# Optimization experiments

Measured on AMD Instinct MI355X. Metric: run time of the kernel, lower is better.

Reference implementation:

```python
import jax, jax.numpy as jnp
import numpy as np


def conv1x1(x, w, b):
    # x: [B,C,H,W], w: [O,C], b: [O] -> [B,O,H,W]
    return jnp.einsum('bchw,oc->bohw', x, w) + b[None, :, None, None]


def setup_inputs() -> dict:
    key = jax.random.key(0)
    ks = jax.random.split(key, 8)
    B, H, W = 32, 64, 64
    PoI_N, PT_feat, T_feat = 128, 64, 32
    poi = jax.random.uniform(ks[0], (B, PoI_N, H, W), dtype=jnp.float32)
    time = jax.random.normal(ks[1], (B, 31, H, W), dtype=jnp.float32)
    s = 0.05
    wm = jax.random.normal(ks[2], (T_feat, 31), dtype=jnp.float32) * s
    bm = jnp.zeros((T_feat,), jnp.float32)
    wf = jax.random.normal(ks[3], (1, T_feat), dtype=jnp.float32) * s
    bf = jnp.zeros((1,), jnp.float32)
    wc = jax.random.normal(ks[4], (PT_feat, PoI_N), dtype=jnp.float32) * s
    bc = jnp.zeros((PT_feat,), jnp.float32)
    return {'poi': poi, 'time': time, 'wm': wm, 'bm': bm, 'wf': wf, 'bf': bf, 'wc': wc, 'bc': bc}


def reference(poi, time, wm, bm, wf, bf, wc, bc):
    # Time_trans: conv1x1 -> relu -> conv1x1 -> relu, out channels = 1
    z = jax.nn.relu(conv1x1(time, wm, bm))
    T_x = jax.nn.relu(conv1x1(z, wf, bf))  # [B,1,H,W]
    # original does a detached CPU tile/multiply: broadcast multiply, no grad through it
    poi_time = jax.lax.stop_gradient(T_x * poi)  # [B,PoI_N,H,W]
    return conv1x1(poi_time, wc, bc)
```

## Files before the change

kernel.cpp:

```cpp
#include <hip/hip_runtime.h>
#include <hip/hip_bf16.h>

typedef short bf16x8 __attribute__((ext_vector_type(8)));
typedef float f32x4  __attribute__((ext_vector_type(4)));
typedef unsigned int u32;
typedef unsigned int u32x4 __attribute__((ext_vector_type(4)));

constexpr int HW = 4096;
constexpr int CT = 31;
constexpr int CZ = 32;
constexpr int CP = 128;
constexpr int CO = 64;

__device__ __forceinline__ u32 f2bfu(float x) {
    __hip_bfloat16 h = __float2bfloat16(x);
    return (u32)*reinterpret_cast<unsigned short*>(&h);
}

__global__ __launch_bounds__(256)
void time_mlp2(const float* __restrict__ tin,
               const float* __restrict__ wm,
               const float* __restrict__ bm,
               const float* __restrict__ wf,
               const float* __restrict__ bf,
               float* __restrict__ tbuf)
{
    const int gid = blockIdx.x * 256 + threadIdx.x;
    const int px  = gid * 2;
    const int b   = px >> 12;
    const float* tp = tin + (size_t)b * CT * HW + (px & (HW - 1));

    float2 tr[CT];
    #pragma unroll
    for (int c = 0; c < CT; ++c)
        tr[c] = *reinterpret_cast<const float2*>(tp + (size_t)c * HW);
    __builtin_amdgcn_sched_barrier(0);

    float ax = bf[0], ay = ax;
    #pragma unroll
    for (int k = 0; k < CZ; ++k) {
        float zx = bm[k], zy = zx;
        #pragma unroll
        for (int c = 0; c < CT; ++c) {
            const float w = wm[k * CT + c];
            zx = fmaf(w, tr[c].x, zx);
            zy = fmaf(w, tr[c].y, zy);
        }
        const float wk = wf[k];
        ax = fmaf(wk, fmaxf(zx, 0.f), ax);
        ay = fmaf(wk, fmaxf(zy, 0.f), ay);
    }
    float2 r; r.x = fmaxf(ax, 0.f); r.y = fmaxf(ay, 0.f);
    *reinterpret_cast<float2*>(tbuf + px) = r;
}

__global__ __launch_bounds__(256)
void poi_gemm_lds(const float* __restrict__ poi,
                  const float* __restrict__ tbuf,
                  const float* __restrict__ wc,
                  const float* __restrict__ bc,
                  float* __restrict__ out)
{
    __shared__ __align__(16) unsigned short s_poi[64 * CP];

    const int tid  = threadIdx.x;
    const int lane = tid & 63;
    const int m    = lane & 15;
    const int g    = lane >> 4;
    const int wid  = tid >> 6;
    const int b    = blockIdx.x >> 6;
    const int px0  = (blockIdx.x & 63) << 6;

    bf16x8 wcf[4];
    #pragma unroll
    for (int kf = 0; kf < 4; ++kf)
      #pragma unroll
      for (int j = 0; j < 8; ++j)
        wcf[kf][j] = (short)f2bfu(wc[(wid * 16 + m) * CP + kf * 32 + g * 8 + j]);
    const float bcf = bc[wid * 16 + m];

    {
        const int p2 = tid & 31;
        const int cg = tid >> 5;
        const float* src = poi + (size_t)b * CP * HW + (size_t)(cg * 16) * HW
                               + px0 + p2 * 2;
        float2 v[16];
        #pragma unroll
        for (int j = 0; j < 16; ++j)
            v[j] = *reinterpret_cast<const float2*>(src + (size_t)j * HW);
        __builtin_amdgcn_sched_barrier(0);

        u32 r0[8], r1[8];
        #pragma unroll
        for (int j = 0; j < 8; ++j) {
            r0[j] = f2bfu(v[2 * j].x) | (f2bfu(v[2 * j + 1].x) << 16);
            r1[j] = f2bfu(v[2 * j].y) | (f2bfu(v[2 * j + 1].y) << 16);
        }
        u32* lds = reinterpret_cast<u32*>(s_poi);
        const int swz = (p2 & 7) << 2;
        const int d0  = (2 * p2) * (CP / 2) + cg * 8;
        const int d1  = d0 + (CP / 2);
        u32x4 a0 = {r0[0], r0[1], r0[2], r0[3]};
        u32x4 a1 = {r0[4], r0[5], r0[6], r0[7]};
        u32x4 b0 = {r1[0], r1[1], r1[2], r1[3]};
        u32x4 b1 = {r1[4], r1[5], r1[6], r1[7]};
        *reinterpret_cast<u32x4*>(lds + ((d0    ) ^ swz)) = a0;
        *reinterpret_cast<u32x4*>(lds + ((d0 + 4) ^ swz)) = a1;
        *reinterpret_cast<u32x4*>(lds + ((d1    ) ^ swz)) = b0;
        *reinterpret_cast<u32x4*>(lds + ((d1 + 4) ^ swz)) = b1;
    }
    __syncthreads();

    const float* tb = tbuf + (size_t)b * HW + px0;
    float* obase = out + (size_t)b * CO * HW + (size_t)(wid * 16 + m) * HW
                       + px0 + g * 4;
    const u32* lds = reinterpret_cast<const u32*>(s_poi);

    #pragma unroll
    for (int t = 0; t < 4; ++t) {
        const int p     = t * 16 + m;
        const int swzr  = ((p >> 1) & 7) << 2;
        const int dbase = p * (CP / 2);

        bf16x8 pfv[4];
        #pragma unroll
        for (int kf = 0; kf < 4; ++kf)
            pfv[kf] = *reinterpret_cast<const bf16x8*>(
                lds + ((dbase + kf * 16 + g * 4) ^ swzr));

        f32x4 a = {0.f, 0.f, 0.f, 0.f};
        #pragma unroll
        for (int kf = 0; kf < 4; ++kf)
            a = __builtin_amdgcn_mfma_f32_16x16x32_bf16(pfv[kf], wcf[kf], a, 0, 0, 0);

        const f32x4 tv = *reinterpret_cast<const f32x4*>(tb + t * 16 + g * 4);
        f32x4 v;
        #pragma unroll
        for (int r = 0; r < 4; ++r) v[r] = fmaf(tv[r], a[r], bcf);
        __builtin_nontemporal_store(v, reinterpret_cast<f32x4*>(obase + t * 16));
    }
}

extern "C" void kernel_launch(void* const* d_in, const int* in_sizes, int n_in,
                              void* d_out, int out_size, void* d_ws, size_t ws_size,
                              hipStream_t stream) {
    const float* poi = (const float*)d_in[0];
    const float* tin = (const float*)d_in[1];
    const float* wm  = (const float*)d_in[2];
    const float* bm  = (const float*)d_in[3];
    const float* wf  = (const float*)d_in[4];
    const float* bf  = (const float*)d_in[5];
    const float* wc  = (const float*)d_in[6];
    const float* bc  = (const float*)d_in[7];
    float* out  = (float*)d_out;
    float* tbuf = (float*)d_ws;

    hipLaunchKernelGGL(time_mlp2, dim3(256), dim3(256), 0, stream,
                       tin, wm, bm, wf, bf, tbuf);
    hipLaunchKernelGGL(poi_gemm_lds, dim3(2048), dim3(256), 0, stream,
                       poi, tbuf, wc, bc, out);
}
```

Measured before the change: 44.53 us.

## Process two pixel strips per block with double-buffered LDS to overlap loads

Each block of the POI GEMM kernel now handles two 64-pixel strips and uses two LDS buffers. The second strip's global loads are issued before the first strip's MFMA compute and stores, so memory latency overlaps with compute. The grid is halved to 1024 blocks. In exchange, LDS use per block doubles, the grid has fewer blocks to hide latency with, and the v[] registers stay live across the compute phase.

```diff
diff --git a/kernel.cpp b/kernel.cpp
--- a/kernel.cpp
+++ b/kernel.cpp
@@ -55,21 +55,21 @@
 }
 
 __global__ __launch_bounds__(256)
-void poi_gemm_lds(const float* __restrict__ poi,
-                  const float* __restrict__ tbuf,
-                  const float* __restrict__ wc,
-                  const float* __restrict__ bc,
-                  float* __restrict__ out)
+void poi_gemm_pipe(const float* __restrict__ poi,
+                   const float* __restrict__ tbuf,
+                   const float* __restrict__ wc,
+                   const float* __restrict__ bc,
+                   float* __restrict__ out)
 {
-    __shared__ __align__(16) unsigned short s_poi[64 * CP];
+    __shared__ __align__(16) unsigned short s_poi[2][64 * CP];
 
     const int tid  = threadIdx.x;
     const int lane = tid & 63;
     const int m    = lane & 15;
     const int g    = lane >> 4;
     const int wid  = tid >> 6;
-    const int b    = blockIdx.x >> 6;
-    const int px0  = (blockIdx.x & 63) << 6;
+    const int p2   = tid & 31;
+    const int cg   = tid >> 5;
 
     bf16x8 wcf[4];
     #pragma unroll
@@ -79,24 +79,25 @@
         wcf[kf][j] = (short)f2bfu(wc[(wid * 16 + m) * CP + kf * 32 + g * 8 + j]);
     const float bcf = bc[wid * 16 + m];
 
-    {
-        const int p2 = tid & 31;
-        const int cg = tid >> 5;
+    const int S0 = blockIdx.x * 2;
+
+    float2 v[16];
+    auto load_strip = [&](int S) {
+        const int b = S >> 6, px0 = (S & 63) << 6;
         const float* src = poi + (size_t)b * CP * HW + (size_t)(cg * 16) * HW
                                + px0 + p2 * 2;
-        float2 v[16];
         #pragma unroll
         for (int j = 0; j < 16; ++j)
             v[j] = *reinterpret_cast<const float2*>(src + (size_t)j * HW);
-        __builtin_amdgcn_sched_barrier(0);
-
+    };
+    auto cvt_write = [&](int buf) {
         u32 r0[8], r1[8];
         #pragma unroll
         for (int j = 0; j < 8; ++j) {
             r0[j] = f2bfu(v[2 * j].x) | (f2bfu(v[2 * j + 1].x) << 16);
             r1[j] = f2bfu(v[2 * j].y) | (f2bfu(v[2 * j + 1].y) << 16);
         }
-        u32* lds = reinterpret_cast<u32*>(s_poi);
+        u32* lds = reinterpret_cast<u32*>(s_poi[buf]);
         const int swz = (p2 & 7) << 2;
         const int d0  = (2 * p2) * (CP / 2) + cg * 8;
         const int d1  = d0 + (CP / 2);
@@ -108,37 +109,48 @@
         *reinterpret_cast<u32x4*>(lds + ((d0 + 4) ^ swz)) = a1;
         *reinterpret_cast<u32x4*>(lds + ((d1    ) ^ swz)) = b0;
         *reinterpret_cast<u32x4*>(lds + ((d1 + 4) ^ swz)) = b1;
-    }
-    __syncthreads();
+    };
+    auto compute_store = [&](int S, int buf) {
+        const int b = S >> 6, px0 = (S & 63) << 6;
+        const float* tb = tbuf + (size_t)b * HW + px0;
+        float* obase = out + (size_t)b * CO * HW + (size_t)(wid * 16 + m) * HW
+                           + px0 + g * 4;
+        const u32* lds = reinterpret_cast<const u32*>(s_poi[buf]);
+        #pragma unroll
+        for (int t = 0; t < 4; ++t) {
+            const int p     = t * 16 + m;
+            const int swzr  = ((p >> 1) & 7) << 2;
+            const int dbase = p * (CP / 2);
+            bf16x8 pfv[4];
+            #pragma unroll
+            for (int kf = 0; kf < 4; ++kf)
+                pfv[kf] = *reinterpret_cast<const bf16x8*>(
+                    lds + ((dbase + kf * 16 + g * 4) ^ swzr));
+            f32x4 a = {0.f, 0.f, 0.f, 0.f};
+            #pragma unroll
+            for (int kf = 0; kf < 4; ++kf)
+                a = __builtin_amdgcn_mfma_f32_16x16x32_bf16(pfv[kf], wcf[kf], a, 0, 0, 0);
+            const f32x4 tv = *reinterpret_cast<const f32x4*>(tb + t * 16 + g * 4);
+            f32x4 r;
+            #pragma unroll
+            for (int q = 0; q < 4; ++q) r[q] = fmaf(tv[q], a[q], bcf);
+            __builtin_nontemporal_store(r, reinterpret_cast<f32x4*>(obase + t * 16));
+        }
+    };
 
-    const float* tb = tbuf + (size_t)b * HW + px0;
-    float* obase = out + (size_t)b * CO * HW + (size_t)(wid * 16 + m) * HW
-                       + px0 + g * 4;
-    const u32* lds = reinterpret_cast<const u32*>(s_poi);
-
-    #pragma unroll
-    for (int t = 0; t < 4; ++t) {
-        const int p     = t * 16 + m;
-        const int swzr  = ((p >> 1) & 7) << 2;
-        const int dbase = p * (CP / 2);
-
-        bf16x8 pfv[4];
-        #pragma unroll
-        for (int kf = 0; kf < 4; ++kf)
-            pfv[kf] = *reinterpret_cast<const bf16x8*>(
-                lds + ((dbase + kf * 16 + g * 4) ^ swzr));
-
-        f32x4 a = {0.f, 0.f, 0.f, 0.f};
-        #pragma unroll
-        for (int kf = 0; kf < 4; ++kf)
-            a = __builtin_amdgcn_mfma_f32_16x16x32_bf16(pfv[kf], wcf[kf], a, 0, 0, 0);
-
-        const f32x4 tv = *reinterpret_cast<const f32x4*>(tb + t * 16 + g * 4);
-        f32x4 v;
-        #pragma unroll
-        for (int r = 0; r < 4; ++r) v[r] = fmaf(tv[r], a[r], bcf);
-        __builtin_nontemporal_store(v, reinterpret_cast<f32x4*>(obase + t * 16));
-    }
+    load_strip(S0);
+    cvt_write(0);
+    load_strip(S0 + 1);
+    __builtin_amdgcn_sched_barrier(0);
+    asm volatile("s_waitcnt lgkmcnt(0)" ::: "memory");
+    __builtin_amdgcn_s_barrier();
+    __builtin_amdgcn_sched_barrier(0);
+    compute_store(S0, 0);
+    cvt_write(1);
+    asm volatile("s_waitcnt lgkmcnt(0)" ::: "memory");
+    __builtin_amdgcn_s_barrier();
+    __builtin_amdgcn_sched_barrier(0);
+    compute_store(S0 + 1, 1);
 }
 
 extern "C" void kernel_launch(void* const* d_in, const int* in_sizes, int n_in,
@@ -157,6 +169,6 @@
 
     hipLaunchKernelGGL(time_mlp2, dim3(256), dim3(256), 0, stream,
                        tin, wm, bm, wf, bf, tbuf);
-    hipLaunchKernelGGL(poi_gemm_lds, dim3(2048), dim3(256), 0, stream,
+    hipLaunchKernelGGL(poi_gemm_pipe, dim3(1024), dim3(256), 0, stream,
                        poi, tbuf, wc, bc, out);
 }
```

Result: no change. 44.64 us (+0.3%).
